# Kernel tuning notes

Hardware: AMD Instinct MI355X
Metric: run time of the kernel (lower is better)

Reference implementation:

```python
import jax, jax.numpy as jnp
import numpy as np

T = 1.0  # temperature (default in original forward)


def setup_inputs() -> dict:
    key = jax.random.key(0)
    k1, k2 = jax.random.split(key)
    N, M, D = 65536, 512, 256
    z = jax.random.normal(k1, (N, D), dtype=jnp.float32)
    e = jax.random.normal(k2, (M, D), dtype=jnp.float32)
    log_sigma = jnp.zeros((1,), dtype=jnp.float32)  # init_log_sigma = 0.0
    return {"z": z, "e": e, "log_sigma": log_sigma}


def reference(z, e, log_sigma):
    N, z_dim = z.shape
    M = e.shape[0]
    # pad N up to a multiple of M (zeros), then view as [B, M, z_dim]
    N_pad = ((N + M - 1) // M) * M
    z = jnp.pad(z, ((0, N_pad - N), (0, 0)))
    zb = z.reshape(-1, M, z_dim)  # [B, M, D]
    # squared euclidean distance via GEMM form: ||z||^2 + ||e||^2 - 2 z.e -> [B, M, M]
    dist = (
        jnp.sum(zb * zb, axis=-1)[:, :, None]
        + jnp.sum(e * e, axis=-1)[None, None, :]
        - 2.0 * jnp.einsum("bmd,kd->bmk", zb, e)
    )
    alpha = -1.0 / (2.0 * jnp.exp(log_sigma[0]) ** 2)
    # logsumexp over the z-block dim (axis=1), mean over codebook dim (axis=1 after reduce)
    loss = -jnp.mean(T * jax.nn.logsumexp(alpha * dist / T, axis=1), axis=1)  # [B]
    loss = loss + 0.5 * z_dim * (2.0 * log_sigma[0] - 1.0) + jnp.log(jnp.float32(M))
    return jnp.mean(loss)
```

## Files before the change

### kernel.cpp

```cpp
#include <hip/hip_runtime.h>
#include <stdint.h>
#include <math.h>

typedef __attribute__((ext_vector_type(8))) short short8;
typedef __attribute__((ext_vector_type(16))) float f32x16;

#define DEVI static __device__ __forceinline__

constexpr int D = 256;
constexpr float LOG2E = 1.4426950408889634f;
constexpr float LN2   = 0.6931471805599453f;
constexpr float SHIFT = 96.0f;

constexpr size_t WS_EIMG  = 0;
constexpr size_t WS_ETERM = 262144;
constexpr size_t WS_WSUM  = 264192;
constexpr size_t WS_PART  = WS_WSUM + 2097152;

DEVI unsigned int f2bf(float f) {
  unsigned int u = __float_as_uint(f);
  return (u + 0x7fffu + ((u >> 16) & 1u)) >> 16;
}
DEVI unsigned int cvtpk(float lo, float hi) {
  unsigned int r;
  asm("v_cvt_pk_bf16_f32 %0, %1, %2" : "=v"(r) : "v"(lo), "v"(hi));
  return r;
}
DEVI float d4(float4 x) { return x.x*x.x + x.y*x.y + x.z*x.z + x.w*x.w; }
DEVI float shflx(float v, int m) { return __shfl_xor(v, m, 64); }

__global__ void prep_e(const float* __restrict__ e, const float* __restrict__ lsp,
                       char* __restrict__ eimg, float* __restrict__ eterm) {
  const int et = blockIdx.x, t = threadIdx.x;
  const int c = t >> 3, o = t & 7;
  const int gc = et * 32 + c;
  const float a = __expf(-2.0f * lsp[0]);
  const float sab = a * LOG2E;
  const float* s = e + (size_t)gc * D + o * 32;
  float sq = 0.0f;
  unsigned int w[16];
#pragma unroll
  for (int i = 0; i < 8; ++i) {
    float4 x = *(const float4*)(s + i * 4);
    sq += d4(x);
    w[2 * i]     = f2bf(sab * x.x) | (f2bf(sab * x.y) << 16);
    w[2 * i + 1] = f2bf(sab * x.z) | (f2bf(sab * x.w) << 16);
  }
  sq += shflx(sq, 1); sq += shflx(sq, 2); sq += shflx(sq, 4);
  char* base = eimg + (size_t)et * 16384;
#pragma unroll
  for (int i = 0; i < 4; ++i) {
    int g = o * 4 + i;
    int phys = (g >> 1) * 1024 + (g & 1) * 512 + c * 16;
    uint4 pk; pk.x = w[4 * i]; pk.y = w[4 * i + 1];
    pk.z = w[4 * i + 2]; pk.w = w[4 * i + 3];
    *(uint4*)(base + phys) = pk;
  }
  if (o == 0) eterm[gc] = -0.5f * a * sq;
}

__global__ __launch_bounds__(512, 4)
void lse_main(const float* __restrict__ z, const char* __restrict__ eimg,
              const float* __restrict__ lsp, float* __restrict__ wsum) {
  __shared__ char  zbuf[32768];
  __shared__ float ztm[64];

  const int tid = threadIdx.x;
  const int wid = tid >> 6, lane = tid & 63;
  const int l31 = lane & 31;
  const int hi  = lane >> 5;
  const int bx = blockIdx.x;
  const int rowblk = bx >> 1, half = bx & 1;
  const float a = __expf(-2.0f * lsp[0]);
  const float ztf = -0.5f * a * LOG2E;

  {
    const int srow = tid >> 4;
    const int gp = (tid & 15) * 2;
    const float* p0 = z + ((size_t)rowblk * 64 + srow) * D + gp * 8;
    const float* p1 = p0 + (size_t)32 * D;
    float4 u0 = *(const float4*)(p0),     u1 = *(const float4*)(p0 + 4);
    float4 u2 = *(const float4*)(p0 + 8), u3 = *(const float4*)(p0 + 12);
    float4 w0 = *(const float4*)(p1),     w1 = *(const float4*)(p1 + 4);
    float4 w2 = *(const float4*)(p1 + 8), w3 = *(const float4*)(p1 + 12);
    float squ = d4(u0) + d4(u1) + d4(u2) + d4(u3);
    float sqw = d4(w0) + d4(w1) + d4(w2) + d4(w3);
    squ += shflx(squ, 1); squ += shflx(squ, 2);
    squ += shflx(squ, 4); squ += shflx(squ, 8);
    sqw += shflx(sqw, 1); sqw += shflx(sqw, 2);
    sqw += shflx(sqw, 4); sqw += shflx(sqw, 8);
    uint4 a0, a1, b0, b1;
    a0.x = cvtpk(u0.x, u0.y); a0.y = cvtpk(u0.z, u0.w);
    a0.z = cvtpk(u1.x, u1.y); a0.w = cvtpk(u1.z, u1.w);
    a1.x = cvtpk(u2.x, u2.y); a1.y = cvtpk(u2.z, u2.w);
    a1.z = cvtpk(u3.x, u3.y); a1.w = cvtpk(u3.z, u3.w);
    b0.x = cvtpk(w0.x, w0.y); b0.y = cvtpk(w0.z, w0.w);
    b0.z = cvtpk(w1.x, w1.y); b0.w = cvtpk(w1.z, w1.w);
    b1.x = cvtpk(w2.x, w2.y); b1.y = cvtpk(w2.z, w2.w);
    b1.z = cvtpk(w3.x, w3.y); b1.w = cvtpk(w3.z, w3.w);
    char* rb = zbuf + srow * 512;
    *(uint4*)(rb + ((gp ^ srow) * 16))               = a0;
    *(uint4*)(rb + (((gp + 1) ^ srow) * 16))         = a1;
    *(uint4*)(rb + 16384 + ((gp ^ srow) * 16))       = b0;
    *(uint4*)(rb + 16384 + (((gp + 1) ^ srow) * 16)) = b1;
    if ((tid & 15) == 0) {
      ztm[srow]      = ztf * squ + SHIFT;
      ztm[32 + srow] = ztf * sqw + SHIFT;
    }
  }
  __syncthreads();

  const char* bp = eimg + (size_t)(half * 8 + wid) * 16384 + (size_t)lane * 16;
  short8 Bq[4];
#pragma unroll
  for (int i = 0; i < 4; ++i) Bq[i] = *(const short8*)(bp + i * 1024);

  f32x16 acc0, acc1;
#pragma unroll
  for (int i = 0; i < 16; ++i) { acc0[i] = 0.f; acc1[i] = 0.f; }
  const int C0 = l31 * 512 + ((hi * 16) ^ (l31 * 16));
  __builtin_amdgcn_s_setprio(1);
#pragma unroll
  for (int s = 0; s < 16; ++s) {
    short8 Bc = Bq[s & 3];
    if (s + 4 < 16) Bq[s & 3] = *(const short8*)(bp + (s + 4) * 1024);
    const int slot = C0 ^ (s * 32);
    short8 A0 = *(const short8*)(zbuf + slot);
    short8 A1 = *(const short8*)(zbuf + slot + 16384);
    acc0 = __builtin_amdgcn_mfma_f32_32x32x16_bf16(A0, Bc, acc0, 0, 0, 0);
    acc1 = __builtin_amdgcn_mfma_f32_32x32x16_bf16(A1, Bc, acc1, 0, 0, 0);
  }
  __builtin_amdgcn_s_setprio(0);

  float s0 = 0.f, s1 = 0.f, s2 = 0.f, s3 = 0.f;
#pragma unroll
  for (int j = 0; j < 4; ++j) {
    float4 z0 = *(const float4*)&ztm[8 * j + 4 * hi];
    float4 z1 = *(const float4*)&ztm[32 + 8 * j + 4 * hi];
    s0 += exp2f(acc0[4 * j]     + z0.x) + exp2f(acc1[4 * j]     + z1.x);
    s1 += exp2f(acc0[4 * j + 1] + z0.y) + exp2f(acc1[4 * j + 1] + z1.y);
    s2 += exp2f(acc0[4 * j + 2] + z0.z) + exp2f(acc1[4 * j + 2] + z1.z);
    s3 += exp2f(acc0[4 * j + 3] + z0.w) + exp2f(acc1[4 * j + 3] + z1.w);
  }
  float sm = (s0 + s1) + (s2 + s3);
  sm += shflx(sm, 32);
  if (hi == 0) {
    const int col = half * 256 + wid * 32 + l31;
    wsum[(size_t)rowblk * 512 + col] = sm;
  }
}

__global__ void merge_b(const float* __restrict__ wsum,
                        const float* __restrict__ eterm, float* __restrict__ partial) {
  __shared__ float sh[512];
  const int b = blockIdx.x, t = threadIdx.x;
  float s = 0.0f;
#pragma unroll
  for (int i = 0; i < 8; ++i)
    s += wsum[(size_t)(8 * b + i) * 512 + t];
  sh[t] = LN2 * (log2f(s) - SHIFT) + eterm[t];
  __syncthreads();
  for (int st = 256; st > 0; st >>= 1) {
    if (t < st) sh[t] += sh[t + st];
    __syncthreads();
  }
  if (t == 0) partial[b] = sh[0];
}

__global__ void final_k(const float* __restrict__ partial,
                        const float* __restrict__ lsp, float* __restrict__ out) {
  __shared__ float sh[128];
  const int t = threadIdx.x;
  sh[t] = partial[t];
  __syncthreads();
  for (int st = 64; st > 0; st >>= 1) {
    if (t < st) sh[t] += sh[t + st];
    __syncthreads();
  }
  if (t == 0) {
    float ls = lsp[0];
    out[0] = -sh[0] / 65536.0f + 128.0f * (2.0f * ls - 1.0f) + logf(512.0f);
  }
}

extern "C" void kernel_launch(void* const* d_in, const int* in_sizes, int n_in,
                              void* d_out, int out_size, void* d_ws, size_t ws_size,
                              hipStream_t stream) {
  const float* z   = (const float*)d_in[0];
  const float* e   = (const float*)d_in[1];
  const float* lsp = (const float*)d_in[2];
  float* out = (float*)d_out;
  char* ws = (char*)d_ws;
  char*  eimg    = ws + WS_EIMG;
  float* eterm   = (float*)(ws + WS_ETERM);
  float* wsum    = (float*)(ws + WS_WSUM);
  float* partial = (float*)(ws + WS_PART);

  prep_e<<<dim3(16), dim3(256), 0, stream>>>(e, lsp, eimg, eterm);
  lse_main<<<dim3(2048), dim3(512), 0, stream>>>(z, eimg, lsp, wsum);
  merge_b<<<dim3(128), dim3(512), 0, stream>>>(wsum, eterm, partial);
  final_k<<<dim3(1), dim3(128), 0, stream>>>(partial, lsp, out);
}
```

Before: 44.05 us.

## Halve workgroup size and give each wave two codebook column tiles

The main kernel now runs 256 threads (4 waves) per block instead of 512, and each wave computes a 64x64 output tile using four MFMA accumulators over two codebook column groups, reusing each A fragment twice. The z staging loop is restructured so each thread loads 32 floats per row across two passes, with the swizzle key adapted. The B fragments are loaded directly inside the loop instead of through a 4-deep register prefetch ring. This halves the number of waves per block and doubles the register accumulators per wave, which may lower occupancy and latency hiding for the global B loads.

```diff
diff --git a/kernel.cpp b/kernel.cpp
--- a/kernel.cpp
+++ b/kernel.cpp
@@ -59,7 +59,7 @@
   if (o == 0) eterm[gc] = -0.5f * a * sq;
 }
 
-__global__ __launch_bounds__(512, 4)
+__global__ __launch_bounds__(256, 4)
 void lse_main(const float* __restrict__ z, const char* __restrict__ eimg,
               const float* __restrict__ lsp, float* __restrict__ wsum) {
   __shared__ char  zbuf[32768];
@@ -74,79 +74,80 @@
   const float a = __expf(-2.0f * lsp[0]);
   const float ztf = -0.5f * a * LOG2E;
 
-  {
-    const int srow = tid >> 4;
-    const int gp = (tid & 15) * 2;
-    const float* p0 = z + ((size_t)rowblk * 64 + srow) * D + gp * 8;
-    const float* p1 = p0 + (size_t)32 * D;
-    float4 u0 = *(const float4*)(p0),     u1 = *(const float4*)(p0 + 4);
-    float4 u2 = *(const float4*)(p0 + 8), u3 = *(const float4*)(p0 + 12);
-    float4 w0 = *(const float4*)(p1),     w1 = *(const float4*)(p1 + 4);
-    float4 w2 = *(const float4*)(p1 + 8), w3 = *(const float4*)(p1 + 12);
-    float squ = d4(u0) + d4(u1) + d4(u2) + d4(u3);
-    float sqw = d4(w0) + d4(w1) + d4(w2) + d4(w3);
-    squ += shflx(squ, 1); squ += shflx(squ, 2);
-    squ += shflx(squ, 4); squ += shflx(squ, 8);
-    sqw += shflx(sqw, 1); sqw += shflx(sqw, 2);
-    sqw += shflx(sqw, 4); sqw += shflx(sqw, 8);
-    uint4 a0, a1, b0, b1;
+#pragma unroll
+  for (int p = 0; p < 2; ++p) {
+    const int srow = p * 32 + (tid >> 3);
+    const int o = tid & 7;
+    const float* src = z + ((size_t)rowblk * 64 + srow) * D + o * 32;
+    float4 u0 = *(const float4*)(src),      u1 = *(const float4*)(src + 4);
+    float4 u2 = *(const float4*)(src + 8),  u3 = *(const float4*)(src + 12);
+    float4 u4 = *(const float4*)(src + 16), u5 = *(const float4*)(src + 20);
+    float4 u6 = *(const float4*)(src + 24), u7 = *(const float4*)(src + 28);
+    float sq = d4(u0) + d4(u1) + d4(u2) + d4(u3) +
+               d4(u4) + d4(u5) + d4(u6) + d4(u7);
+    sq += shflx(sq, 1); sq += shflx(sq, 2); sq += shflx(sq, 4);
+    uint4 a0, a1, a2, a3;
     a0.x = cvtpk(u0.x, u0.y); a0.y = cvtpk(u0.z, u0.w);
     a0.z = cvtpk(u1.x, u1.y); a0.w = cvtpk(u1.z, u1.w);
     a1.x = cvtpk(u2.x, u2.y); a1.y = cvtpk(u2.z, u2.w);
     a1.z = cvtpk(u3.x, u3.y); a1.w = cvtpk(u3.z, u3.w);
-    b0.x = cvtpk(w0.x, w0.y); b0.y = cvtpk(w0.z, w0.w);
-    b0.z = cvtpk(w1.x, w1.y); b0.w = cvtpk(w1.z, w1.w);
-    b1.x = cvtpk(w2.x, w2.y); b1.y = cvtpk(w2.z, w2.w);
-    b1.z = cvtpk(w3.x, w3.y); b1.w = cvtpk(w3.z, w3.w);
+    a2.x = cvtpk(u4.x, u4.y); a2.y = cvtpk(u4.z, u4.w);
+    a2.z = cvtpk(u5.x, u5.y); a2.w = cvtpk(u5.z, u5.w);
+    a3.x = cvtpk(u6.x, u6.y); a3.y = cvtpk(u6.z, u6.w);
+    a3.z = cvtpk(u7.x, u7.y); a3.w = cvtpk(u7.z, u7.w);
     char* rb = zbuf + srow * 512;
-    *(uint4*)(rb + ((gp ^ srow) * 16))               = a0;
-    *(uint4*)(rb + (((gp + 1) ^ srow) * 16))         = a1;
-    *(uint4*)(rb + 16384 + ((gp ^ srow) * 16))       = b0;
-    *(uint4*)(rb + 16384 + (((gp + 1) ^ srow) * 16)) = b1;
-    if ((tid & 15) == 0) {
-      ztm[srow]      = ztf * squ + SHIFT;
-      ztm[32 + srow] = ztf * sqw + SHIFT;
-    }
+    const int key = srow & 31;
+    *(uint4*)(rb + (((4 * o + 0) ^ key) * 16)) = a0;
+    *(uint4*)(rb + (((4 * o + 1) ^ key) * 16)) = a1;
+    *(uint4*)(rb + (((4 * o + 2) ^ key) * 16)) = a2;
+    *(uint4*)(rb + (((4 * o + 3) ^ key) * 16)) = a3;
+    if (o == 0) ztm[srow] = ztf * sq + SHIFT;
   }
   __syncthreads();
 
-  const char* bp = eimg + (size_t)(half * 8 + wid) * 16384 + (size_t)lane * 16;
-  short8 Bq[4];
-#pragma unroll
-  for (int i = 0; i < 4; ++i) Bq[i] = *(const short8*)(bp + i * 1024);
-
-  f32x16 acc0, acc1;
-#pragma unroll
-  for (int i = 0; i < 16; ++i) { acc0[i] = 0.f; acc1[i] = 0.f; }
+  const char* bp0 = eimg + (size_t)(half * 8 + 2 * wid) * 16384 + (size_t)lane * 16;
+  const char* bp1 = bp0 + 16384;
+
+  f32x16 acc00, acc01, acc10, acc11;
+#pragma unroll
+  for (int i = 0; i < 16; ++i) { acc00[i] = 0.f; acc01[i] = 0.f;
+                                 acc10[i] = 0.f; acc11[i] = 0.f; }
   const int C0 = l31 * 512 + ((hi * 16) ^ (l31 * 16));
   __builtin_amdgcn_s_setprio(1);
 #pragma unroll
   for (int s = 0; s < 16; ++s) {
-    short8 Bc = Bq[s & 3];
-    if (s + 4 < 16) Bq[s & 3] = *(const short8*)(bp + (s + 4) * 1024);
     const int slot = C0 ^ (s * 32);
     short8 A0 = *(const short8*)(zbuf + slot);
     short8 A1 = *(const short8*)(zbuf + slot + 16384);
-    acc0 = __builtin_amdgcn_mfma_f32_32x32x16_bf16(A0, Bc, acc0, 0, 0, 0);
-    acc1 = __builtin_amdgcn_mfma_f32_32x32x16_bf16(A1, Bc, acc1, 0, 0, 0);
+    short8 B0 = *(const short8*)(bp0 + s * 1024);
+    short8 B1 = *(const short8*)(bp1 + s * 1024);
+    acc00 = __builtin_amdgcn_mfma_f32_32x32x16_bf16(A0, B0, acc00, 0, 0, 0);
+    acc10 = __builtin_amdgcn_mfma_f32_32x32x16_bf16(A1, B0, acc10, 0, 0, 0);
+    acc01 = __builtin_amdgcn_mfma_f32_32x32x16_bf16(A0, B1, acc01, 0, 0, 0);
+    acc11 = __builtin_amdgcn_mfma_f32_32x32x16_bf16(A1, B1, acc11, 0, 0, 0);
   }
   __builtin_amdgcn_s_setprio(0);
 
-  float s0 = 0.f, s1 = 0.f, s2 = 0.f, s3 = 0.f;
+  float t0s = 0.f, t1s = 0.f;
 #pragma unroll
   for (int j = 0; j < 4; ++j) {
     float4 z0 = *(const float4*)&ztm[8 * j + 4 * hi];
     float4 z1 = *(const float4*)&ztm[32 + 8 * j + 4 * hi];
-    s0 += exp2f(acc0[4 * j]     + z0.x) + exp2f(acc1[4 * j]     + z1.x);
-    s1 += exp2f(acc0[4 * j + 1] + z0.y) + exp2f(acc1[4 * j + 1] + z1.y);
-    s2 += exp2f(acc0[4 * j + 2] + z0.z) + exp2f(acc1[4 * j + 2] + z1.z);
-    s3 += exp2f(acc0[4 * j + 3] + z0.w) + exp2f(acc1[4 * j + 3] + z1.w);
-  }
-  float sm = (s0 + s1) + (s2 + s3);
-  sm += shflx(sm, 32);
+    t0s += exp2f(acc00[4 * j]     + z0.x) + exp2f(acc10[4 * j]     + z1.x)
+         + exp2f(acc00[4 * j + 1] + z0.y) + exp2f(acc10[4 * j + 1] + z1.y)
+         + exp2f(acc00[4 * j + 2] + z0.z) + exp2f(acc10[4 * j + 2] + z1.z)
+         + exp2f(acc00[4 * j + 3] + z0.w) + exp2f(acc10[4 * j + 3] + z1.w);
+    t1s += exp2f(acc01[4 * j]     + z0.x) + exp2f(acc11[4 * j]     + z1.x)
+         + exp2f(acc01[4 * j + 1] + z0.y) + exp2f(acc11[4 * j + 1] + z1.y)
+         + exp2f(acc01[4 * j + 2] + z0.z) + exp2f(acc11[4 * j + 2] + z1.z)
+         + exp2f(acc01[4 * j + 3] + z0.w) + exp2f(acc11[4 * j + 3] + z1.w);
+  }
+  t0s += shflx(t0s, 32);
+  t1s += shflx(t1s, 32);
   if (hi == 0) {
-    const int col = half * 256 + wid * 32 + l31;
-    wsum[(size_t)rowblk * 512 + col] = sm;
+    const int colbase = half * 256 + 2 * wid * 32;
+    wsum[(size_t)rowblk * 512 + colbase + l31]      = t0s;
+    wsum[(size_t)rowblk * 512 + colbase + 32 + l31] = t1s;
   }
 }
 
@@ -197,7 +198,7 @@
   float* partial = (float*)(ws + WS_PART);
 
   prep_e<<<dim3(16), dim3(256), 0, stream>>>(e, lsp, eimg, eterm);
-  lse_main<<<dim3(2048), dim3(512), 0, stream>>>(z, eimg, lsp, wsum);
+  lse_main<<<dim3(2048), dim3(256), 0, stream>>>(z, eimg, lsp, wsum);
   merge_b<<<dim3(128), dim3(512), 0, stream>>>(wsum, eterm, partial);
   final_k<<<dim3(1), dim3(128), 0, stream>>>(partial, lsp, out);
 }
```

Measured after the change: 46.77 us. +6.2%, slower.
